# Kernel optimization log

Hardware: AMD Instinct MI355X
Metric: run time of the kernel (lower is better)

Reference implementation:

```python
import jax, jax.numpy as jnp
import numpy as np

HEADS = 16
DIM_HEAD = 64
MAX_FREQ = 256.0  # lucidrains RotaryEmbedding(freqs_for='pixel', max_freq=256)


def axial_freqs(H, W, dim_head):
    # per-axis rotary dim = dim_head // 2 (RotaryEmbedding(dim=head_dim//2))
    d = dim_head // 2
    base = jnp.linspace(1.0, MAX_FREQ / 2.0, d // 2) * jnp.pi  # (d/2,)

    def axis(n):
        pos = jnp.linspace(-1.0, 1.0, n)              # pixel positions
        f = pos[:, None] * base                        # (n, d/2)
        return jnp.repeat(f, 2, axis=-1)               # (n, d) interleaved pairs

    fh = jnp.broadcast_to(axis(H)[:, None, :], (H, W, d))
    fw = jnp.broadcast_to(axis(W)[None, :, :], (H, W, d))
    return jnp.concatenate([fh, fw], axis=-1)          # (H, W, dim_head)


def apply_rope(t, freqs):
    # t: (B,T,H,W,h,d); freqs: (H,W,d)
    f = freqs[:, :, None, :]                           # broadcast over heads
    x = t.reshape(t.shape[:-1] + (t.shape[-1] // 2, 2))
    x1, x2 = x[..., 0], x[..., 1]
    rot = jnp.stack([-x2, x1], axis=-1).reshape(t.shape)  # rotate_half (interleaved)
    return t * jnp.cos(f) + rot * jnp.sin(f)


def setup_inputs() -> dict:
    key = jax.random.key(0)
    k1, k2, k3 = jax.random.split(key, 3)
    B, T, H, W, D = 1, 8, 32, 32, 1024
    inner = HEADS * DIM_HEAD
    x = jax.random.normal(k1, (B, T, H, W, D), dtype=jnp.float32)
    Wqkv = jax.random.normal(k2, (D, 3 * inner), dtype=jnp.float32) * 0.02
    Wout = jax.random.normal(k3, (inner, D), dtype=jnp.float32) * 0.02
    bout = jnp.zeros((D,), dtype=jnp.float32)
    return {"x": x, "Wqkv": Wqkv, "Wout": Wout, "bout": bout}


def reference(x, Wqkv, Wout, bout):
    B, T, H, W, D = x.shape
    qkv = x @ Wqkv                                     # (B,T,H,W,3*inner)
    q, k, v = jnp.split(qkv, 3, axis=-1)
    shp = (B, T, H, W, HEADS, DIM_HEAD)
    q, k, v = q.reshape(shp), k.reshape(shp), v.reshape(shp)
    freqs = axial_freqs(H, W, DIM_HEAD)
    q = apply_rope(q, freqs)
    k = apply_rope(k, freqs)
    S = H * W
    q = q.reshape(B * T, S, HEADS, DIM_HEAD)
    k = k.reshape(B * T, S, HEADS, DIM_HEAD)
    v = v.reshape(B * T, S, HEADS, DIM_HEAD)
    scale = 1.0 / np.sqrt(DIM_HEAD).astype(np.float32)
    att = jnp.einsum('bshd,bthd->bhst', q, k) * scale  # (BT, h, S, S)
    att = jax.nn.softmax(att, axis=-1)
    o = jnp.einsum('bhst,bthd->bshd', att, v)          # (BT, S, h, d)
    o = o.reshape(B, T, H, W, HEADS * DIM_HEAD)
    return o @ Wout + bout
```

## Files before the change

kernel.cpp:

```cpp
#include <hip/hip_runtime.h>
#include <math.h>

#define DMODEL 1024
#define NQKV   3072
#define SEQ    1024
#define NH     16
#define DH     64
#define HS     (SEQ*DH)
constexpr float PI_F   = 3.14159265358979323846f;
constexpr float LOG2E  = 1.44269504088896f;

typedef _Float16 half8   __attribute__((ext_vector_type(8)));
typedef _Float16 half4   __attribute__((ext_vector_type(4)));
typedef float    floatx4 __attribute__((ext_vector_type(4)));

__device__ __forceinline__ void gload_lds16(const _Float16* g, _Float16* l) {
    __builtin_amdgcn_global_load_lds(
        (const __attribute__((address_space(1))) unsigned int*)g,
        (__attribute__((address_space(3)))       unsigned int*)l,
        16, 0, 0);
}

__global__ __launch_bounds__(256) void cvt_f16(
    const float* __restrict__ in, _Float16* __restrict__ out, int n)
{
    int i = (blockIdx.x*256 + threadIdx.x)*8;
    if (i >= n) return;
    float4 a = *(const float4*)(in + i);
    float4 b = *(const float4*)(in + i + 4);
    half8 h;
    h[0]=(_Float16)a.x; h[1]=(_Float16)a.y; h[2]=(_Float16)a.z; h[3]=(_Float16)a.w;
    h[4]=(_Float16)b.x; h[5]=(_Float16)b.y; h[6]=(_Float16)b.z; h[7]=(_Float16)b.w;
    *(half8*)(out + i) = h;
}

__global__ __launch_bounds__(256) void tr_cvt(
    const float* __restrict__ in, _Float16* __restrict__ out, int R, int C)
{
    __shared__ float T[32][33];
    const int bx = blockIdx.x, by = blockIdx.y;
    const int tx = threadIdx.x & 31, ty = threadIdx.x >> 5;
#pragma unroll
    for (int i = 0; i < 4; ++i)
        T[ty + i*8][tx] = in[(size_t)(by*32 + ty + i*8)*C + bx*32 + tx];
    __syncthreads();
#pragma unroll
    for (int i = 0; i < 4; ++i)
        out[(size_t)(bx*32 + ty + i*8)*R + by*32 + tx] = (_Float16)T[tx][ty + i*8];
}

__global__ __launch_bounds__(256) void gemm1_f16(
    const _Float16* __restrict__ A, const _Float16* __restrict__ Bt,
    _Float16* __restrict__ C, int M, int N, int K)
{
    __shared__ _Float16 As[128*32];
    __shared__ _Float16 Bs[128*32];
    const int tid = threadIdx.x;
    const int w = tid >> 6, lane = tid & 63, quad = lane >> 4, l = lane & 15;
    const int wm = (w & 1)*64, wn = (w >> 1)*64;
    const int m0 = blockIdx.y*128, n0 = blockIdx.x*128;

    const _Float16* a0 = A  + (size_t)(m0 + w*32      + (lane>>2))*K + (lane&3)*8;
    const _Float16* a1 = A  + (size_t)(m0 + w*32 + 16 + (lane>>2))*K + (lane&3)*8;
    const _Float16* b0 = Bt + (size_t)(n0 + w*32      + (lane>>2))*K + (lane&3)*8;
    const _Float16* b1 = Bt + (size_t)(n0 + w*32 + 16 + (lane>>2))*K + (lane&3)*8;
    _Float16* lA0 = As + w*1024;
    _Float16* lA1 = As + w*1024 + 512;
    _Float16* lB0 = Bs + w*1024;
    _Float16* lB1 = Bs + w*1024 + 512;

    floatx4 acc[4][4];
#pragma unroll
    for (int i = 0; i < 4; ++i)
#pragma unroll
        for (int j = 0; j < 4; ++j)
#pragma unroll
            for (int r = 0; r < 4; ++r) acc[i][j][r] = 0.f;

    for (int k0 = 0; k0 < K; k0 += 32) {
        __syncthreads();
        gload_lds16(a0, lA0); gload_lds16(a1, lA1);
        gload_lds16(b0, lB0); gload_lds16(b1, lB1);
        a0 += 32; a1 += 32; b0 += 32; b1 += 32;
        __syncthreads();
        half8 bf[4];
#pragma unroll
        for (int nt = 0; nt < 4; ++nt)
            bf[nt] = *(half8*)&Bs[(wn + nt*16 + l)*32 + quad*8];
#pragma unroll
        for (int mt = 0; mt < 4; ++mt) {
            half8 af = *(half8*)&As[(wm + mt*16 + l)*32 + quad*8];
#pragma unroll
            for (int nt = 0; nt < 4; ++nt)
                acc[mt][nt] = __builtin_amdgcn_mfma_f32_16x16x32_f16(af, bf[nt], acc[mt][nt], 0, 0, 0);
        }
    }
#pragma unroll
    for (int mt = 0; mt < 4; ++mt)
#pragma unroll
        for (int r = 0; r < 4; ++r) {
            size_t row = m0 + wm + mt*16 + quad*4 + r;
#pragma unroll
            for (int nt = 0; nt < 4; ++nt)
                C[row*N + n0 + wn + nt*16 + l] = (_Float16)acc[mt][nt][r];
        }
}

__global__ __launch_bounds__(256) void gemm2_f16(
    const _Float16* __restrict__ A, const _Float16* __restrict__ Bt,
    const float* __restrict__ bias, float* __restrict__ C, int M, int N, int K)
{
    __shared__ _Float16 As[128*32];
    __shared__ _Float16 Bs[128*32];
    const int tid = threadIdx.x;
    const int w = tid >> 6, lane = tid & 63, quad = lane >> 4, l = lane & 15;
    const int wm = (w & 1)*64, wn = (w >> 1)*64;
    const int m0 = blockIdx.y*128, n0 = blockIdx.x*128;

    const _Float16* a0 = A  + (size_t)(m0 + w*32      + (lane>>2))*K + (lane&3)*8;
    const _Float16* a1 = A  + (size_t)(m0 + w*32 + 16 + (lane>>2))*K + (lane&3)*8;
    const _Float16* b0 = Bt + (size_t)(n0 + w*32      + (lane>>2))*K + (lane&3)*8;
    const _Float16* b1 = Bt + (size_t)(n0 + w*32 + 16 + (lane>>2))*K + (lane&3)*8;
    _Float16* lA0 = As + w*1024;
    _Float16* lA1 = As + w*1024 + 512;
    _Float16* lB0 = Bs + w*1024;
    _Float16* lB1 = Bs + w*1024 + 512;

    floatx4 acc[4][4];
#pragma unroll
    for (int i = 0; i < 4; ++i)
#pragma unroll
        for (int j = 0; j < 4; ++j)
#pragma unroll
            for (int r = 0; r < 4; ++r) acc[i][j][r] = 0.f;

    for (int k0 = 0; k0 < K; k0 += 32) {
        __syncthreads();
        gload_lds16(a0, lA0); gload_lds16(a1, lA1);
        gload_lds16(b0, lB0); gload_lds16(b1, lB1);
        a0 += 32; a1 += 32; b0 += 32; b1 += 32;
        __syncthreads();
        half8 bf[4];
#pragma unroll
        for (int nt = 0; nt < 4; ++nt)
            bf[nt] = *(half8*)&Bs[(wn + nt*16 + l)*32 + quad*8];
#pragma unroll
        for (int mt = 0; mt < 4; ++mt) {
            half8 af = *(half8*)&As[(wm + mt*16 + l)*32 + quad*8];
#pragma unroll
            for (int nt = 0; nt < 4; ++nt)
                acc[mt][nt] = __builtin_amdgcn_mfma_f32_16x16x32_f16(af, bf[nt], acc[mt][nt], 0, 0, 0);
        }
    }
#pragma unroll
    for (int mt = 0; mt < 4; ++mt)
#pragma unroll
        for (int r = 0; r < 4; ++r) {
            size_t row = m0 + wm + mt*16 + quad*4 + r;
#pragma unroll
            for (int nt = 0; nt < 4; ++nt) {
                int col = n0 + wn + nt*16 + l;
                C[row*N + col] = acc[mt][nt][r] + bias[col];
            }
        }
}

__global__ __launch_bounds__(256) void rope_scatter(
    const _Float16* __restrict__ qkv,
    _Float16* __restrict__ qw, _Float16* __restrict__ kw,
    _Float16* __restrict__ vt)
{
    const int sc = blockIdx.x;
    const int bh = blockIdx.y;
    const int bt = bh >> 4, head = bh & 15;
    const int s0 = sc*64;
    const int tid = threadIdx.x;
    const int d0 = (tid & 7)*8;

    __shared__ _Float16 T[64][80];

#pragma unroll
    for (int half = 0; half < 2; ++half) {
        const int r = (tid >> 3) + half*32;
        const int s = s0 + r;
        const _Float16* src = qkv + (size_t)(bt*SEQ + s)*NQKV + head*DH + d0;
        half8 hq = *(const half8*)(src);
        half8 hk = *(const half8*)(src + DMODEL);
        half8 hv = *(const half8*)(src + 2*DMODEL);
        float fq[8], fk[8];
#pragma unroll
        for (int j = 0; j < 8; ++j) { fq[j] = (float)hq[j]; fk[j] = (float)hk[j]; }
        const int hp = s >> 5, wp = s & 31;
        const float ph = -1.0f + hp*(2.0f/31.0f);
        const float pw = -1.0f + wp*(2.0f/31.0f);
#pragma unroll
        for (int p = 0; p < 4; ++p) {
            int pg = (d0 >> 1) + p;
            float pos = (pg < 16) ? ph : pw;
            int   gi  = (pg < 16) ? pg : (pg - 16);
            float th  = pos * ((1.0f + gi*(127.0f/15.0f)) * PI_F);
            float sn, cs;
            sincosf(th, &sn, &cs);
            float q1 = fq[2*p], q2 = fq[2*p+1];
            fq[2*p]   = q1*cs - q2*sn;
            fq[2*p+1] = q2*cs + q1*sn;
            float k1 = fk[2*p], k2 = fk[2*p+1];
            fk[2*p]   = k1*cs - k2*sn;
            fk[2*p+1] = k2*cs + k1*sn;
        }
        half8 oq, ok;
        const float qsc = 0.125f * LOG2E;
#pragma unroll
        for (int j = 0; j < 8; ++j) {
            oq[j] = (_Float16)(fq[j]*qsc);
            ok[j] = (_Float16)fk[j];
        }
        *(half8*)(qw + (size_t)bh*HS + (size_t)s*DH + d0) = oq;
        *(half8*)(kw + (size_t)bh*HS + (size_t)s*DH + d0) = ok;
#pragma unroll
        for (int j = 0; j < 8; ++j) T[d0 + j][r] = hv[j];
    }
    __syncthreads();
    const int d = tid >> 2, so = (tid & 3)*16;
    half8 v0 = *(half8*)&T[d][so];
    half8 v1 = *(half8*)&T[d][so + 8];
    _Float16* dst = vt + (size_t)bh*HS + (size_t)d*SEQ + s0 + so;
    *(half8*)dst       = v0;
    *(half8*)(dst + 8) = v1;
}

#define BC  64
#define LDH 68

__global__ __launch_bounds__(256) void attn_mfma(
    const _Float16* __restrict__ qw, const _Float16* __restrict__ kw,
    const _Float16* __restrict__ vt, _Float16* __restrict__ om)
{
    const int qc = blockIdx.x;
    const int bh = blockIdx.y;
    const int tid  = threadIdx.x;
    const int w    = tid >> 6;
    const int lane = tid & 63;
    const int quad = lane >> 4;
    const int l    = lane & 15;

    __shared__ _Float16 Ks[2][BC][LDH];
    __shared__ _Float16 Vs[2][DH][LDH];
    __shared__ _Float16 Ps[4][32][LDH];
    __shared__ float    Ls[4][32];

    const _Float16* qp = qw + (size_t)bh*HS + (size_t)(qc*128 + w*32)*DH;
    const _Float16* kp = kw + (size_t)bh*HS;
    const _Float16* vp = vt + (size_t)bh*HS;

    half8 qf[2][2];
#pragma unroll
    for (int qt = 0; qt < 2; ++qt) {
        qf[qt][0] = *(const half8*)(qp + (size_t)(qt*16 + l)*DH + quad*8);
        qf[qt][1] = *(const half8*)(qp + (size_t)(qt*16 + l)*DH + quad*8 + 32);
    }

    const int rs = tid >> 3;
    const int cs = (tid & 7)*8;

    half8 kr0 = *(const half8*)(kp + (size_t)rs*DH + cs);
    half8 kr1 = *(const half8*)(kp + (size_t)(rs+32)*DH + cs);
    half8 vr0 = *(const half8*)(vp + (size_t)rs*SEQ + cs);
    half8 vr1 = *(const half8*)(vp + (size_t)(rs+32)*SEQ + cs);
    *(half8*)&Ks[0][rs][cs]    = kr0;
    *(half8*)&Ks[0][rs+32][cs] = kr1;
    *(half8*)&Vs[0][rs][cs]    = vr0;
    *(half8*)&Vs[0][rs+32][cs] = vr1;

    floatx4 Of[2][4];
#pragma unroll
    for (int qt = 0; qt < 2; ++qt)
#pragma unroll
        for (int dt = 0; dt < 4; ++dt)
#pragma unroll
            for (int r = 0; r < 4; ++r) Of[qt][dt][r] = 0.f;
    float lsum[2] = {0.f, 0.f};

    __syncthreads();

    for (int kc = 0; kc < SEQ/BC; ++kc) {
        const int cur = kc & 1;
        if (kc < SEQ/BC - 1) {
            const _Float16* kn = kp + (size_t)(kc+1)*BC*DH;
            const _Float16* vn = vp + (size_t)(kc+1)*BC;
            kr0 = *(const half8*)(kn + (size_t)rs*DH + cs);
            kr1 = *(const half8*)(kn + (size_t)(rs+32)*DH + cs);
            vr0 = *(const half8*)(vn + (size_t)rs*SEQ + cs);
            vr1 = *(const half8*)(vn + (size_t)(rs+32)*SEQ + cs);
        }

        floatx4 Sf[2][4];
#pragma unroll
        for (int kg = 0; kg < 4; ++kg) {
            half8 af0 = *(half8*)&Ks[cur][kg*16 + l][quad*8];
            half8 af1 = *(half8*)&Ks[cur][kg*16 + l][quad*8 + 32];
#pragma unroll
            for (int qt = 0; qt < 2; ++qt) {
                floatx4 a;
#pragma unroll
                for (int r = 0; r < 4; ++r) a[r] = 0.f;
                a = __builtin_amdgcn_mfma_f32_16x16x32_f16(af0, qf[qt][0], a, 0, 0, 0);
                a = __builtin_amdgcn_mfma_f32_16x16x32_f16(af1, qf[qt][1], a, 0, 0, 0);
                Sf[qt][kg] = a;
            }
        }
#pragma unroll
        for (int qt = 0; qt < 2; ++qt)
#pragma unroll
            for (int kg = 0; kg < 4; ++kg) {
                half4 p4;
#pragma unroll
                for (int r = 0; r < 4; ++r) {
                    float p = __builtin_amdgcn_exp2f(Sf[qt][kg][r]);
                    lsum[qt] += p;
                    p4[r] = (_Float16)p;
                }
                *(half4*)&Ps[w][qt*16 + l][kg*16 + quad*4] = p4;
            }
        half8 pa[2][2];
#pragma unroll
        for (int qt = 0; qt < 2; ++qt) {
            pa[qt][0] = *(half8*)&Ps[w][qt*16 + l][quad*8];
            pa[qt][1] = *(half8*)&Ps[w][qt*16 + l][quad*8 + 32];
        }
#pragma unroll
        for (int dt = 0; dt < 4; ++dt) {
            half8 vb0 = *(half8*)&Vs[cur][dt*16 + l][quad*8];
            half8 vb1 = *(half8*)&Vs[cur][dt*16 + l][quad*8 + 32];
#pragma unroll
            for (int qt = 0; qt < 2; ++qt) {
                Of[qt][dt] = __builtin_amdgcn_mfma_f32_16x16x32_f16(pa[qt][0], vb0, Of[qt][dt], 0, 0, 0);
                Of[qt][dt] = __builtin_amdgcn_mfma_f32_16x16x32_f16(pa[qt][1], vb1, Of[qt][dt], 0, 0, 0);
            }
        }

        if (kc < SEQ/BC - 1) {
            *(half8*)&Ks[1-cur][rs][cs]    = kr0;
            *(half8*)&Ks[1-cur][rs+32][cs] = kr1;
            *(half8*)&Vs[1-cur][rs][cs]    = vr0;
            *(half8*)&Vs[1-cur][rs+32][cs] = vr1;
        }
        __syncthreads();
    }

#pragma unroll
    for (int qt = 0; qt < 2; ++qt) {
        lsum[qt] += __shfl_xor(lsum[qt], 16);
        lsum[qt] += __shfl_xor(lsum[qt], 32);
        if (quad == 0) Ls[w][qt*16 + l] = lsum[qt];
    }
    const int bt = bh >> 4, head = bh & 15;
    _Float16* opf = om + (size_t)(bt*SEQ + qc*128 + w*32)*DMODEL + head*DH;
#pragma unroll
    for (int qt = 0; qt < 2; ++qt) {
        float inv[4];
#pragma unroll
        for (int r = 0; r < 4; ++r) inv[r] = 1.0f / Ls[w][qt*16 + quad*4 + r];
#pragma unroll
        for (int dt = 0; dt < 4; ++dt)
#pragma unroll
            for (int r = 0; r < 4; ++r)
                opf[(size_t)(qt*16 + quad*4 + r)*DMODEL + dt*16 + l] =
                    (_Float16)(Of[qt][dt][r]*inv[r]);
    }
}

extern "C" void kernel_launch(void* const* d_in, const int* in_sizes, int n_in,
                              void* d_out, int out_size, void* d_ws, size_t ws_size,
                              hipStream_t stream)
{
    const float* x    = (const float*)d_in[0];
    const float* Wqkv = (const float*)d_in[1];
    const float* Wout = (const float*)d_in[2];
    const float* bout = (const float*)d_in[3];
    float* out = (float*)d_out;

    _Float16* ws   = (_Float16*)d_ws;
    _Float16* Xh   = ws;
    _Float16* Wqkt = ws + 8388608;
    _Float16* Wot  = ws + 11534336;
    _Float16* qkvt = ws + 12582912;
    _Float16* qw   = ws + 37748736;
    _Float16* kw   = ws + 46137344;
    _Float16* vt   = ws + 54525952;
    _Float16* om   = qkvt;

    hipLaunchKernelGGL(cvt_f16, dim3(4096), dim3(256), 0, stream,
                       x, Xh, 8388608);
    hipLaunchKernelGGL(tr_cvt, dim3(96, 32), dim3(256), 0, stream,
                       Wqkv, Wqkt, 1024, 3072);
    hipLaunchKernelGGL(tr_cvt, dim3(32, 32), dim3(256), 0, stream,
                       Wout, Wot, 1024, 1024);
    hipLaunchKernelGGL(gemm1_f16, dim3(24, 64), dim3(256), 0, stream,
                       Xh, Wqkt, qkvt, 8192, NQKV, DMODEL);
    hipLaunchKernelGGL(rope_scatter, dim3(16, 128), dim3(256), 0, stream,
                       qkvt, qw, kw, vt);
    hipLaunchKernelGGL(attn_mfma, dim3(8, 128), dim3(256), 0, stream,
                       qw, kw, vt, om);
    hipLaunchKernelGGL(gemm2_f16, dim3(8, 64), dim3(256), 0, stream,
                       om, Wot, bout, out, 8192, DMODEL, DMODEL);
}
```

Baseline: 281.6 us.

## Rewrite QKV GEMM with 256x256 tiles, double-buffered LDS and swizzle

The QKV projection GEMM moves from 128x128x32 tiles with 4 waves to 256x256x64 tiles with 8 waves. It double-buffers LDS so global-to-LDS loads for the next k-tile overlap the MFMA work on the current one. It also XOR-swizzles the LDS layout to avoid bank conflicts, remaps block IDs in an XCD-aware way, and uses setprio around the MFMA clusters. The aim is more data reuse per tile and hiding load latency, at the cost of 128KB of LDS per block, high register pressure from 32 accumulators, and a grid of only 384 blocks.

```diff
diff --git a/kernel.cpp b/kernel.cpp
--- a/kernel.cpp
+++ b/kernel.cpp
@@ -49,54 +49,140 @@
         out[(size_t)(bx*32 + ty + i*8)*R + by*32 + tx] = (_Float16)T[tx][ty + i*8];
 }
 
-__global__ __launch_bounds__(256) void gemm1_f16(
+#define G1_BM 256
+#define G1_BN 256
+#define G1_BK 64
+
+__global__ __launch_bounds__(512) void gemm1_f16(
     const _Float16* __restrict__ A, const _Float16* __restrict__ Bt,
     _Float16* __restrict__ C, int M, int N, int K)
 {
-    __shared__ _Float16 As[128*32];
-    __shared__ _Float16 Bs[128*32];
-    const int tid = threadIdx.x;
-    const int w = tid >> 6, lane = tid & 63, quad = lane >> 4, l = lane & 15;
-    const int wm = (w & 1)*64, wn = (w >> 1)*64;
-    const int m0 = blockIdx.y*128, n0 = blockIdx.x*128;
-
-    const _Float16* a0 = A  + (size_t)(m0 + w*32      + (lane>>2))*K + (lane&3)*8;
-    const _Float16* a1 = A  + (size_t)(m0 + w*32 + 16 + (lane>>2))*K + (lane&3)*8;
-    const _Float16* b0 = Bt + (size_t)(n0 + w*32      + (lane>>2))*K + (lane&3)*8;
-    const _Float16* b1 = Bt + (size_t)(n0 + w*32 + 16 + (lane>>2))*K + (lane&3)*8;
-    _Float16* lA0 = As + w*1024;
-    _Float16* lA1 = As + w*1024 + 512;
-    _Float16* lB0 = Bs + w*1024;
-    _Float16* lB1 = Bs + w*1024 + 512;
-
-    floatx4 acc[4][4];
-#pragma unroll
-    for (int i = 0; i < 4; ++i)
+    __shared__ _Float16 As[2][G1_BM*G1_BK] __attribute__((aligned(16)));
+    __shared__ _Float16 Bs[2][G1_BN*G1_BK] __attribute__((aligned(16)));
+
+    const int tid  = threadIdx.x;
+    const int w    = tid >> 6, lane = tid & 63, quad = lane >> 4, l = lane & 15;
+    const int wm   = (w >> 2)*128, wn = (w & 3)*64;
+
+    int bid = blockIdx.y*gridDim.x + blockIdx.x;
+    const int per = (gridDim.x*gridDim.y) >> 3;
+    bid = (bid & 7)*per + (bid >> 3);
+    const int bx = bid % gridDim.x, by = bid / gridDim.x;
+    const int m0 = by*G1_BM, n0 = bx*G1_BN;
+
+    const int sr  = tid >> 3;
+    const int scg = (tid & 7) ^ (sr & 7);
+    const _Float16* ga = A  + (size_t)(m0 + sr)*K + scg*8;
+    const _Float16* gb = Bt + (size_t)(n0 + sr)*K + scg*8;
+
+#define G1_STAGE_A(buf, kt, s) \
+    gload_lds16(ga + (size_t)(s)*64*K + (size_t)(kt)*G1_BK, \
+                &As[buf][(s)*4096 + w*512])
+#define G1_STAGE_B(buf, kt, s) \
+    gload_lds16(gb + (size_t)(s)*64*K + (size_t)(kt)*G1_BK, \
+                &Bs[buf][(s)*4096 + w*512])
+#define G1_RD_A(buf, mt, kh) \
+    (*(half8*)&As[buf][(wm + (mt)*16 + l)*64 + ((((kh)*4 + quad) ^ (l & 7))*8)])
+#define G1_RD_B(buf, nt, kh) \
+    (*(half8*)&Bs[buf][(wn + (nt)*16 + l)*64 + ((((kh)*4 + quad) ^ (l & 7))*8)])
+
+    floatx4 acc[8][4];
+#pragma unroll
+    for (int i = 0; i < 8; ++i)
 #pragma unroll
         for (int j = 0; j < 4; ++j)
 #pragma unroll
             for (int r = 0; r < 4; ++r) acc[i][j][r] = 0.f;
 
-    for (int k0 = 0; k0 < K; k0 += 32) {
-        __syncthreads();
-        gload_lds16(a0, lA0); gload_lds16(a1, lA1);
-        gload_lds16(b0, lB0); gload_lds16(b1, lB1);
-        a0 += 32; a1 += 32; b0 += 32; b1 += 32;
-        __syncthreads();
-        half8 bf[4];
-#pragma unroll
-        for (int nt = 0; nt < 4; ++nt)
-            bf[nt] = *(half8*)&Bs[(wn + nt*16 + l)*32 + quad*8];
-#pragma unroll
-        for (int mt = 0; mt < 4; ++mt) {
-            half8 af = *(half8*)&As[(wm + mt*16 + l)*32 + quad*8];
-#pragma unroll
-            for (int nt = 0; nt < 4; ++nt)
-                acc[mt][nt] = __builtin_amdgcn_mfma_f32_16x16x32_f16(af, bf[nt], acc[mt][nt], 0, 0, 0);
-        }
-    }
-#pragma unroll
-    for (int mt = 0; mt < 4; ++mt)
+#pragma unroll
+    for (int s = 0; s < 4; ++s) G1_STAGE_A(0, 0, s);
+#pragma unroll
+    for (int s = 0; s < 4; ++s) G1_STAGE_B(0, 0, s);
+    asm volatile("s_waitcnt vmcnt(0)" ::: "memory");
+    __builtin_amdgcn_s_barrier();
+    __builtin_amdgcn_sched_barrier(0);
+
+    const int KT = K / G1_BK;
+    for (int kt = 0; kt < KT; ++kt) {
+        const int cur = kt & 1, nxt = cur ^ 1;
+        const bool pf = (kt + 1 < KT);
+        half8 a0[4], a1[4], b0[2], b1[2];
+
+#pragma unroll
+        for (int mt = 0; mt < 4; ++mt) { a0[mt] = G1_RD_A(cur, mt, 0); a1[mt] = G1_RD_A(cur, mt, 1); }
+#pragma unroll
+        for (int nt = 0; nt < 2; ++nt) { b0[nt] = G1_RD_B(cur, nt, 0); b1[nt] = G1_RD_B(cur, nt, 1); }
+        if (pf) { G1_STAGE_A(nxt, kt+1, 0); G1_STAGE_A(nxt, kt+1, 1);
+                  G1_STAGE_B(nxt, kt+1, 0); G1_STAGE_B(nxt, kt+1, 1); }
+        __builtin_amdgcn_s_barrier();
+        asm volatile("s_waitcnt lgkmcnt(0)" ::: "memory");
+        __builtin_amdgcn_sched_barrier(0);
+        __builtin_amdgcn_s_setprio(1);
+#pragma unroll
+        for (int mt = 0; mt < 4; ++mt)
+#pragma unroll
+            for (int nt = 0; nt < 2; ++nt) {
+                acc[mt][nt] = __builtin_amdgcn_mfma_f32_16x16x32_f16(a0[mt], b0[nt], acc[mt][nt], 0, 0, 0);
+                acc[mt][nt] = __builtin_amdgcn_mfma_f32_16x16x32_f16(a1[mt], b1[nt], acc[mt][nt], 0, 0, 0);
+            }
+        __builtin_amdgcn_s_setprio(0);
+        __builtin_amdgcn_s_barrier();
+
+#pragma unroll
+        for (int nt = 0; nt < 2; ++nt) { b0[nt] = G1_RD_B(cur, nt+2, 0); b1[nt] = G1_RD_B(cur, nt+2, 1); }
+        if (pf) { G1_STAGE_A(nxt, kt+1, 2); G1_STAGE_A(nxt, kt+1, 3);
+                  G1_STAGE_B(nxt, kt+1, 2); G1_STAGE_B(nxt, kt+1, 3); }
+        __builtin_amdgcn_s_barrier();
+        asm volatile("s_waitcnt lgkmcnt(0)" ::: "memory");
+        __builtin_amdgcn_sched_barrier(0);
+        __builtin_amdgcn_s_setprio(1);
+#pragma unroll
+        for (int mt = 0; mt < 4; ++mt)
+#pragma unroll
+            for (int nt = 0; nt < 2; ++nt) {
+                acc[mt][nt+2] = __builtin_amdgcn_mfma_f32_16x16x32_f16(a0[mt], b0[nt], acc[mt][nt+2], 0, 0, 0);
+                acc[mt][nt+2] = __builtin_amdgcn_mfma_f32_16x16x32_f16(a1[mt], b1[nt], acc[mt][nt+2], 0, 0, 0);
+            }
+        __builtin_amdgcn_s_setprio(0);
+        __builtin_amdgcn_s_barrier();
+
+#pragma unroll
+        for (int mt = 0; mt < 4; ++mt) { a0[mt] = G1_RD_A(cur, mt+4, 0); a1[mt] = G1_RD_A(cur, mt+4, 1); }
+        __builtin_amdgcn_s_barrier();
+        asm volatile("s_waitcnt lgkmcnt(0)" ::: "memory");
+        __builtin_amdgcn_sched_barrier(0);
+        __builtin_amdgcn_s_setprio(1);
+#pragma unroll
+        for (int mt = 0; mt < 4; ++mt)
+#pragma unroll
+            for (int nt = 0; nt < 2; ++nt) {
+                acc[mt+4][nt+2] = __builtin_amdgcn_mfma_f32_16x16x32_f16(a0[mt], b0[nt], acc[mt+4][nt+2], 0, 0, 0);
+                acc[mt+4][nt+2] = __builtin_amdgcn_mfma_f32_16x16x32_f16(a1[mt], b1[nt], acc[mt+4][nt+2], 0, 0, 0);
+            }
+        __builtin_amdgcn_s_setprio(0);
+        __builtin_amdgcn_s_barrier();
+
+#pragma unroll
+        for (int nt = 0; nt < 2; ++nt) { b0[nt] = G1_RD_B(cur, nt, 0); b1[nt] = G1_RD_B(cur, nt, 1); }
+        __builtin_amdgcn_s_barrier();
+        asm volatile("s_waitcnt lgkmcnt(0)" ::: "memory");
+        __builtin_amdgcn_sched_barrier(0);
+        __builtin_amdgcn_s_setprio(1);
+#pragma unroll
+        for (int mt = 0; mt < 4; ++mt)
+#pragma unroll
+            for (int nt = 0; nt < 2; ++nt) {
+                acc[mt+4][nt] = __builtin_amdgcn_mfma_f32_16x16x32_f16(a0[mt], b0[nt], acc[mt+4][nt], 0, 0, 0);
+                acc[mt+4][nt] = __builtin_amdgcn_mfma_f32_16x16x32_f16(a1[mt], b1[nt], acc[mt+4][nt], 0, 0, 0);
+            }
+        __builtin_amdgcn_s_setprio(0);
+        asm volatile("s_waitcnt vmcnt(0)" ::: "memory");
+        __builtin_amdgcn_s_barrier();
+        __builtin_amdgcn_sched_barrier(0);
+    }
+
+#pragma unroll
+    for (int mt = 0; mt < 8; ++mt)
 #pragma unroll
         for (int r = 0; r < 4; ++r) {
             size_t row = m0 + wm + mt*16 + quad*4 + r;
@@ -104,6 +190,10 @@
             for (int nt = 0; nt < 4; ++nt)
                 C[row*N + n0 + wn + nt*16 + l] = (_Float16)acc[mt][nt][r];
         }
+#undef G1_STAGE_A
+#undef G1_STAGE_B
+#undef G1_RD_A
+#undef G1_RD_B
 }
 
 __global__ __launch_bounds__(256) void gemm2_f16(
@@ -396,7 +486,7 @@
                        Wqkv, Wqkt, 1024, 3072);
     hipLaunchKernelGGL(tr_cvt, dim3(32, 32), dim3(256), 0, stream,
                        Wout, Wot, 1024, 1024);
-    hipLaunchKernelGGL(gemm1_f16, dim3(24, 64), dim3(256), 0, stream,
+    hipLaunchKernelGGL(gemm1_f16, dim3(12, 32), dim3(512), 0, stream,
                        Xh, Wqkt, qkvt, 8192, NQKV, DMODEL);
     hipLaunchKernelGGL(rope_scatter, dim3(16, 128), dim3(256), 0, stream,
                        qkvt, qw, kw, vt);
```

After: 271.4 us. 3.6% less time.
